# Optimization experiments

Measured on AMD Instinct MI355X. Metric: run time of the kernel, lower is better.

Reference implementation:

```python
import jax, jax.numpy as jnp
import numpy as np
from jax import lax

B, S, DIMS, T, K = 4, 4096, 2048, 10, 2


def setup_inputs() -> dict:
    key = jax.random.key(0)
    ks = jax.random.split(key, 4)
    scale = 1.0 / np.sqrt(DIMS)
    x = jax.random.normal(ks[0], (B, S, DIMS), dtype=jnp.float32)
    W_cls = jax.random.normal(ks[1], (DIMS, T), dtype=jnp.float32) * scale
    W_sparse = jax.random.normal(ks[2], (DIMS, T), dtype=jnp.float32) * scale
    W_gates = jax.random.normal(ks[3], (DIMS, T), dtype=jnp.float32) * scale
    return {
        "x": x,
        "W_cls": W_cls, "b_cls": jnp.zeros((T,), jnp.float32),
        "W_sparse": W_sparse, "b_sparse": jnp.zeros((T,), jnp.float32),
        "W_gates": W_gates, "b_gates": jnp.zeros((T,), jnp.float32),
        "alpha": jnp.ones((1,), jnp.float32),
    }


def reference(x, W_cls, b_cls, W_sparse, b_sparse, W_gates, b_gates, alpha):
    # soft routing: softmax classifier over num_types
    soft_types = jax.nn.softmax(jnp.einsum("bsd,dt->bst", x, W_cls) + b_cls, axis=-1)
    # sparse routing: top-k over logits, softmax over the k kept logits,
    # scattered back into a dense [B,S,T] gate vector (zeros elsewhere)
    logits = jnp.einsum("bsd,dt->bst", x, W_sparse) + b_sparse
    top_v, top_i = lax.top_k(logits, K)                      # [B,S,K]
    sparse_g = jax.nn.softmax(top_v, axis=-1)                # [B,S,K]
    # scatter via one-hot (K and T are tiny)
    sparse_types = jnp.sum(jax.nn.one_hot(top_i, T, dtype=x.dtype) * sparse_g[..., None], axis=-2)  # [B,S,T]
    # per-type sigmoid gates: batched single matmul == stack of Linear(dims,1)+Sigmoid
    gates = jax.nn.sigmoid(jnp.einsum("bsd,dt->bst", x, W_gates) + b_gates)  # [B,S,T]
    a = jax.nn.sigmoid(alpha)                                # [1], broadcasts
    mixed_types = a * sparse_types + (1.0 - a) * soft_types  # [B,S,T]
    # original: gates stacked as [B,S,1,T], mixed unsqueezed to [B,S,1,T], sum over T -> [B,S,1]
    return jnp.sum(gates * mixed_types, axis=-1, keepdims=True)
```

## Files before the change

kernel.cpp:

```cpp
#include <hip/hip_runtime.h>
#include <math.h>
#include <stdint.h>


#define NROWS   16384
#define DIMS_   2048
#define TT      10
#define PITCH   132

typedef __attribute__((ext_vector_type(8))) short short8;
typedef __attribute__((ext_vector_type(4))) float f32x4;

__device__ __forceinline__ unsigned short bf16_rne(float f) {
    unsigned int u = __float_as_uint(f);
    unsigned int r = u + 0x7fffu + ((u >> 16) & 1u);
    return (unsigned short)(r >> 16);
}

__global__ __launch_bounds__(256)
void tgate_k0(const float* __restrict__ W_cls,
              const float* __restrict__ W_sparse,
              const float* __restrict__ W_gates,
              unsigned short* __restrict__ frag)
{
    int t = blockIdx.x * 256 + threadIdx.x;
    int K0   = t >> 7;
    int nt   = (t >> 6) & 1;
    int lane = t & 63;
    int n  = nt * 16 + (lane & 15);
    int kb = K0 * 32 + (lane >> 4) * 8;
    short8 hi, lo;
    #pragma unroll
    for (int j = 0; j < 8; ++j) {
        int k = kb + j;
        float w = 0.0f;
        if (n < 10)      w = W_cls[k * TT + n];
        else if (n < 20) w = W_sparse[k * TT + n - 10];
        else if (n < 30) w = W_gates[k * TT + n - 20];
        unsigned short h = bf16_rne(w);
        float back = __uint_as_float(((unsigned int)h) << 16);
        hi[j] = (short)h;
        lo[j] = (short)bf16_rne(w - back);
    }
    short8* fv = reinterpret_cast<short8*>(frag);
    fv[(K0 * 4 + nt * 2 + 0) * 64 + lane] = hi;
    fv[(K0 * 4 + nt * 2 + 1) * 64 + lane] = lo;
}

__global__ __launch_bounds__(256)
void tgate_k1(const float* __restrict__ x,
              const unsigned short* __restrict__ frag,
              const float* __restrict__ b_cls,
              const float* __restrict__ b_sparse,
              const float* __restrict__ b_gates,
              const float* __restrict__ alpha,
              float* __restrict__ out)
{
    __shared__ float lds[4][16 * PITCH];

    const int tid   = threadIdx.x;
    const int lane  = tid & 63;
    const int wv    = __builtin_amdgcn_readfirstlane(tid >> 6);
    const int row0  = blockIdx.x * 16;
    const int m     = lane & 15;
    const int quad  = lane >> 4;

    float* L = lds[wv];
    const int rs = lane >> 5;
    const int cs = (lane & 31) * 4;
    const float4* x4 = reinterpret_cast<const float4*>(x);
    const int cb = wv * 512;

    float4 pre[8];
    #pragma unroll
    for (int t = 0; t < 8; ++t)
        pre[t] = x4[(size_t)(row0 + 2 * t + rs) * 512 + ((cb + cs) >> 2)];

    const short8* fv = reinterpret_cast<const short8*>(frag);
    f32x4 acc[2][2];
    #pragma unroll
    for (int h = 0; h < 2; ++h) {
        acc[h][0] = (f32x4){0.f, 0.f, 0.f, 0.f};
        acc[h][1] = (f32x4){0.f, 0.f, 0.f, 0.f};
    }

    #pragma unroll
    for (int c = 0; c < 4; ++c) {
        #pragma unroll
        for (int t = 0; t < 8; ++t)
            *reinterpret_cast<float4*>(&L[(2 * t + rs) * PITCH + cs]) = pre[t];
        if (c < 3) {
            #pragma unroll
            for (int t = 0; t < 8; ++t)
                pre[t] = x4[(size_t)(row0 + 2 * t + rs) * 512
                            + ((cb + (c + 1) * 128 + cs) >> 2)];
        }
        const int h = c >> 1;
        const int s = 2 * wv + h;
        #pragma unroll
        for (int ksl = 0; ksl < 4; ++ksl) {
            const int K0 = s * 8 + (c & 1) * 4 + ksl;
            const float* src = &L[m * PITCH + ksl * 32 + quad * 8];
            float4 b0 = *reinterpret_cast<const float4*>(src);
            float4 b1 = *reinterpret_cast<const float4*>(src + 4);
            float f[8] = {b0.x, b0.y, b0.z, b0.w, b1.x, b1.y, b1.z, b1.w};
            short8 ah, al;
            #pragma unroll
            for (int j = 0; j < 8; ++j) {
                unsigned short hh = bf16_rne(f[j]);
                float back = __uint_as_float(((unsigned int)hh) << 16);
                ah[j] = (short)hh;
                al[j] = (short)bf16_rne(f[j] - back);
            }
            short8 fh0 = fv[(K0 * 4 + 0) * 64 + lane];
            short8 fl0 = fv[(K0 * 4 + 1) * 64 + lane];
            short8 fh1 = fv[(K0 * 4 + 2) * 64 + lane];
            short8 fl1 = fv[(K0 * 4 + 3) * 64 + lane];
            acc[h][0] = __builtin_amdgcn_mfma_f32_16x16x32_bf16(ah, fh0, acc[h][0], 0, 0, 0);
            acc[h][0] = __builtin_amdgcn_mfma_f32_16x16x32_bf16(al, fh0, acc[h][0], 0, 0, 0);
            acc[h][0] = __builtin_amdgcn_mfma_f32_16x16x32_bf16(ah, fl0, acc[h][0], 0, 0, 0);
            acc[h][1] = __builtin_amdgcn_mfma_f32_16x16x32_bf16(ah, fh1, acc[h][1], 0, 0, 0);
            acc[h][1] = __builtin_amdgcn_mfma_f32_16x16x32_bf16(al, fh1, acc[h][1], 0, 0, 0);
            acc[h][1] = __builtin_amdgcn_mfma_f32_16x16x32_bf16(ah, fl1, acc[h][1], 0, 0, 0);
        }
    }

    float* red = &lds[0][0];
    __syncthreads();
    #pragma unroll
    for (int h = 0; h < 2; ++h) {
        int s = 2 * wv + h;
        #pragma unroll
        for (int r = 0; r < 4; ++r) {
            int row = quad * 4 + r;
            red[(s * 16 + row) * 33 + m]      = acc[h][0][r];
            red[(s * 16 + row) * 33 + m + 16] = acc[h][1][r];
        }
    }
    __syncthreads();

    float* fold = red + 8 * 16 * 33;
    #pragma unroll
    for (int u = 0; u < 2; ++u) {
        int i = tid * 2 + u;
        int row = i >> 5, j = i & 31;
        float a = 0.0f;
        #pragma unroll
        for (int s = 0; s < 8; ++s) a += red[(s * 16 + row) * 33 + j];
        fold[row * 33 + j] = a;
    }
    __syncthreads();

    if (tid < 16) {
        const float* l = &fold[tid * 33];
        float lc[TT], lsp[TT], g[TT];
        #pragma unroll
        for (int t = 0; t < TT; ++t) {
            lc[t]  = l[t]      + b_cls[t];
            lsp[t] = l[10 + t] + b_sparse[t];
            float lg = l[20 + t] + b_gates[t];
            g[t] = 1.0f / (1.0f + __expf(-lg));
        }
        float mm = lc[0];
        #pragma unroll
        for (int t = 1; t < TT; ++t) mm = fmaxf(mm, lc[t]);
        float esum = 0.0f, gdot = 0.0f;
        #pragma unroll
        for (int t = 0; t < TT; ++t) {
            float e = __expf(lc[t] - mm);
            esum += e;
            gdot = fmaf(g[t], e, gdot);
        }
        float v1 = lsp[0], v2 = -1e30f, gv1 = g[0], gv2 = 0.0f;
        #pragma unroll
        for (int t = 1; t < TT; ++t) {
            if (lsp[t] > v1)      { v2 = v1; gv2 = gv1; v1 = lsp[t]; gv1 = g[t]; }
            else if (lsp[t] > v2) { v2 = lsp[t]; gv2 = g[t]; }
        }
        float s1 = 1.0f / (1.0f + __expf(v2 - v1));
        float s2 = 1.0f - s1;
        float a  = 1.0f / (1.0f + __expf(-alpha[0]));
        float sparse_dot = fmaf(gv1, s1, gv2 * s2);
        out[row0 + tid] = fmaf(a, sparse_dot, (1.0f - a) * (gdot / esum));
    }
}

extern "C" void kernel_launch(void* const* d_in, const int* in_sizes, int n_in,
                              void* d_out, int out_size, void* d_ws, size_t ws_size,
                              hipStream_t stream) {
    const float* x        = (const float*)d_in[0];
    const float* W_cls    = (const float*)d_in[1];
    const float* b_cls    = (const float*)d_in[2];
    const float* W_sparse = (const float*)d_in[3];
    const float* b_sparse = (const float*)d_in[4];
    const float* W_gates  = (const float*)d_in[5];
    const float* b_gates  = (const float*)d_in[6];
    const float* alpha    = (const float*)d_in[7];
    float* out = (float*)d_out;

    unsigned short* frag = (unsigned short*)d_ws;

    tgate_k0<<<dim3(32), dim3(256), 0, stream>>>(W_cls, W_sparse, W_gates, frag);
    tgate_k1<<<dim3(NROWS / 16), dim3(256), 0, stream>>>(x, frag, b_cls, b_sparse,
                                                         b_gates, alpha, out);
}
```

Measured before the change: 209.0 us.

## Stream x into LDS with direct global-to-LDS loads and double buffering

Replaces the register-staged prefetch of x (global load into registers, then ds_write to padded LDS) with __builtin_amdgcn_global_load_lds DMA-style loads into two per-wave LDS buffers of 64-column chunks, using s_waitcnt vmcnt to overlap the next chunk's load with MFMA compute on the current one. This removes the VGPR round-trip and LDS store instructions and shrinks register pressure. The risks are the hand-coded waitcnt encodings, the sched_barriers, and the new LDS layout (4 rows per 260-float segment), which must stay correct. The final reduction still reuses the same LDS, which is now smaller.

Result: no change. 210.4 us (+0.7%).

```diff
diff --git a/kernel.cpp b/kernel.cpp
--- a/kernel.cpp
+++ b/kernel.cpp
@@ -6,7 +6,6 @@
 #define NROWS   16384
 #define DIMS_   2048
 #define TT      10
-#define PITCH   132
 
 typedef __attribute__((ext_vector_type(8))) short short8;
 typedef __attribute__((ext_vector_type(4))) float f32x4;
@@ -47,6 +46,54 @@
     fv[(K0 * 4 + nt * 2 + 1) * 64 + lane] = lo;
 }
 
+__device__ __forceinline__ void issue_chunk(const float* __restrict__ x,
+                                            float* bufbase, int row0, int lane,
+                                            int colf0)
+{
+    #pragma unroll
+    for (int t = 0; t < 4; ++t) {
+        const float* gp = x + (size_t)(row0 + 4 * t + (lane >> 4)) * DIMS_
+                            + colf0 + (lane & 15) * 4;
+        __builtin_amdgcn_global_load_lds(
+            (const __attribute__((address_space(1))) void*)gp,
+            (__attribute__((address_space(3))) void*)(bufbase + t * 260),
+            16, 0, 0);
+    }
+}
+
+__device__ __forceinline__ void compute_chunk(const float* Lbuf,
+                                              const short8* __restrict__ fv,
+                                              int K0b, int lane, int m, int quad,
+                                              f32x4& accA, f32x4& accB)
+{
+    #pragma unroll
+    for (int ksl = 0; ksl < 2; ++ksl) {
+        const int K0 = K0b + ksl;
+        const float* src = Lbuf + (m >> 2) * 260 + (m & 3) * 64 + ksl * 32 + quad * 8;
+        float4 b0 = *reinterpret_cast<const float4*>(src);
+        float4 b1 = *reinterpret_cast<const float4*>(src + 4);
+        float f[8] = {b0.x, b0.y, b0.z, b0.w, b1.x, b1.y, b1.z, b1.w};
+        short8 ah, al;
+        #pragma unroll
+        for (int j = 0; j < 8; ++j) {
+            unsigned short hh = bf16_rne(f[j]);
+            float back = __uint_as_float(((unsigned int)hh) << 16);
+            ah[j] = (short)hh;
+            al[j] = (short)bf16_rne(f[j] - back);
+        }
+        short8 fh0 = fv[(K0 * 4 + 0) * 64 + lane];
+        short8 fl0 = fv[(K0 * 4 + 1) * 64 + lane];
+        short8 fh1 = fv[(K0 * 4 + 2) * 64 + lane];
+        short8 fl1 = fv[(K0 * 4 + 3) * 64 + lane];
+        accA = __builtin_amdgcn_mfma_f32_16x16x32_bf16(ah, fh0, accA, 0, 0, 0);
+        accA = __builtin_amdgcn_mfma_f32_16x16x32_bf16(al, fh0, accA, 0, 0, 0);
+        accA = __builtin_amdgcn_mfma_f32_16x16x32_bf16(ah, fl0, accA, 0, 0, 0);
+        accB = __builtin_amdgcn_mfma_f32_16x16x32_bf16(ah, fh1, accB, 0, 0, 0);
+        accB = __builtin_amdgcn_mfma_f32_16x16x32_bf16(al, fh1, accB, 0, 0, 0);
+        accB = __builtin_amdgcn_mfma_f32_16x16x32_bf16(ah, fl1, accB, 0, 0, 0);
+    }
+}
+
 __global__ __launch_bounds__(256)
 void tgate_k1(const float* __restrict__ x,
               const unsigned short* __restrict__ frag,
@@ -56,7 +103,7 @@
               const float* __restrict__ alpha,
               float* __restrict__ out)
 {
-    __shared__ float lds[4][16 * PITCH];
+    __shared__ alignas(16) float lds[4][2][1040];
 
     const int tid   = threadIdx.x;
     const int lane  = tid & 63;
@@ -64,19 +111,12 @@
     const int row0  = blockIdx.x * 16;
     const int m     = lane & 15;
     const int quad  = lane >> 4;
-
-    float* L = lds[wv];
-    const int rs = lane >> 5;
-    const int cs = (lane & 31) * 4;
-    const float4* x4 = reinterpret_cast<const float4*>(x);
-    const int cb = wv * 512;
-
-    float4 pre[8];
-    #pragma unroll
-    for (int t = 0; t < 8; ++t)
-        pre[t] = x4[(size_t)(row0 + 2 * t + rs) * 512 + ((cb + cs) >> 2)];
-
+    const int cbase = wv * 512;
+
+    float* B0 = &lds[wv][0][0];
+    float* B1 = &lds[wv][1][0];
     const short8* fv = reinterpret_cast<const short8*>(frag);
+
     f32x4 acc[2][2];
     #pragma unroll
     for (int h = 0; h < 2; ++h) {
@@ -84,48 +124,30 @@
         acc[h][1] = (f32x4){0.f, 0.f, 0.f, 0.f};
     }
 
-    #pragma unroll
+    __builtin_amdgcn_sched_barrier(0);
+    issue_chunk(x, B0, row0, lane, cbase + 0 * 64);
+    issue_chunk(x, B1, row0, lane, cbase + 1 * 64);
+
     for (int c = 0; c < 4; ++c) {
-        #pragma unroll
-        for (int t = 0; t < 8; ++t)
-            *reinterpret_cast<float4*>(&L[(2 * t + rs) * PITCH + cs]) = pre[t];
-        if (c < 3) {
-            #pragma unroll
-            for (int t = 0; t < 8; ++t)
-                pre[t] = x4[(size_t)(row0 + 2 * t + rs) * 512
-                            + ((cb + (c + 1) * 128 + cs) >> 2)];
-        }
-        const int h = c >> 1;
-        const int s = 2 * wv + h;
-        #pragma unroll
-        for (int ksl = 0; ksl < 4; ++ksl) {
-            const int K0 = s * 8 + (c & 1) * 4 + ksl;
-            const float* src = &L[m * PITCH + ksl * 32 + quad * 8];
-            float4 b0 = *reinterpret_cast<const float4*>(src);
-            float4 b1 = *reinterpret_cast<const float4*>(src + 4);
-            float f[8] = {b0.x, b0.y, b0.z, b0.w, b1.x, b1.y, b1.z, b1.w};
-            short8 ah, al;
-            #pragma unroll
-            for (int j = 0; j < 8; ++j) {
-                unsigned short hh = bf16_rne(f[j]);
-                float back = __uint_as_float(((unsigned int)hh) << 16);
-                ah[j] = (short)hh;
-                al[j] = (short)bf16_rne(f[j] - back);
-            }
-            short8 fh0 = fv[(K0 * 4 + 0) * 64 + lane];
-            short8 fl0 = fv[(K0 * 4 + 1) * 64 + lane];
-            short8 fh1 = fv[(K0 * 4 + 2) * 64 + lane];
-            short8 fl1 = fv[(K0 * 4 + 3) * 64 + lane];
-            acc[h][0] = __builtin_amdgcn_mfma_f32_16x16x32_bf16(ah, fh0, acc[h][0], 0, 0, 0);
-            acc[h][0] = __builtin_amdgcn_mfma_f32_16x16x32_bf16(al, fh0, acc[h][0], 0, 0, 0);
-            acc[h][0] = __builtin_amdgcn_mfma_f32_16x16x32_bf16(ah, fl0, acc[h][0], 0, 0, 0);
-            acc[h][1] = __builtin_amdgcn_mfma_f32_16x16x32_bf16(ah, fh1, acc[h][1], 0, 0, 0);
-            acc[h][1] = __builtin_amdgcn_mfma_f32_16x16x32_bf16(al, fh1, acc[h][1], 0, 0, 0);
-            acc[h][1] = __builtin_amdgcn_mfma_f32_16x16x32_bf16(ah, fl1, acc[h][1], 0, 0, 0);
-        }
-    }
-
-    float* red = &lds[0][0];
+        __builtin_amdgcn_s_waitcnt(0x0F74);
+        float* buf = (c & 1) ? B1 : B0;
+        compute_chunk(buf, fv, 16 * wv + 2 * c, lane, m, quad, acc[0][0], acc[0][1]);
+        __builtin_amdgcn_sched_barrier(0);
+        issue_chunk(x, buf, row0, lane, cbase + (c + 2) * 64);
+    }
+    for (int c = 4; c < 6; ++c) {
+        __builtin_amdgcn_s_waitcnt(0x0F74);
+        float* buf = (c & 1) ? B1 : B0;
+        compute_chunk(buf, fv, 16 * wv + 2 * c, lane, m, quad, acc[1][0], acc[1][1]);
+        __builtin_amdgcn_sched_barrier(0);
+        issue_chunk(x, buf, row0, lane, cbase + (c + 2) * 64);
+    }
+    __builtin_amdgcn_s_waitcnt(0x0F74);
+    compute_chunk(B0, fv, 16 * wv + 12, lane, m, quad, acc[1][0], acc[1][1]);
+    __builtin_amdgcn_s_waitcnt(0x0F70);
+    compute_chunk(B1, fv, 16 * wv + 14, lane, m, quad, acc[1][0], acc[1][1]);
+
+    float* red = &lds[0][0][0];
     __syncthreads();
     #pragma unroll
     for (int h = 0; h < 2; ++h) {
```
